# Performance work log

Hardware: AMD Instinct MI355X
Metric: run time of the kernel (lower is better)

The kernel has to match this reference:

```python
import jax, jax.numpy as jnp
import numpy as np

OUT_H, OUT_W = 7, 7
SPATIAL_SCALE = 0.25
SAMPLING_RATIO = 2


def setup_inputs() -> dict:
    key = jax.random.key(0)
    kf, kb, kc, ks = jax.random.split(key, 4)
    B, C, H, W = 2, 256, 200, 200
    N, IMG = 1000, 800.0
    features = jax.random.normal(kf, (B, C, H, W), jnp.float32)
    bidx = jax.random.randint(kb, (N,), 0, B).astype(jnp.float32)
    ctr = jax.random.uniform(kc, (N, 2)) * IMG            # box centers in image coords
    size = jax.random.uniform(ks, (N, 2)) * 256.0 + 16.0  # box sizes 16..272 px
    x1y1 = jnp.clip(ctr - size / 2, 0.0, IMG)
    x2y2 = jnp.clip(ctr + size / 2, 0.0, IMG)
    rois = jnp.concatenate(
        [bidx[:, None], x1y1[:, 0:1], x1y1[:, 1:2], x2y2[:, 0:1], x2y2[:, 1:2]], axis=1
    )
    return {"features": features, "rois": rois}


def _roi_align(features, rois):
    # torchvision.ops.roi_align semantics (aligned=False), fully vectorized over ROIs.
    B, C, H, W = features.shape
    N = rois.shape[0]
    ph, pw, ratio, scale = OUT_H, OUT_W, SAMPLING_RATIO, SPATIAL_SCALE
    b = rois[:, 0].astype(jnp.int32)
    x1, y1, x2, y2 = (rois[:, i] * scale for i in (1, 2, 3, 4))
    roi_w = jnp.maximum(x2 - x1, 1.0)
    roi_h = jnp.maximum(y2 - y1, 1.0)
    bin_w = roi_w / pw
    bin_h = roi_h / ph
    # sample coordinate s within bin p: y1 + (p*ratio + i + 0.5) * bin_h / ratio
    sy = jnp.arange(ph * ratio, dtype=features.dtype)
    sx = jnp.arange(pw * ratio, dtype=features.dtype)
    y = y1[:, None] + (sy[None, :] + 0.5) * (bin_h[:, None] / ratio)  # (N, Sy)
    x = x1[:, None] + (sx[None, :] + 0.5) * (bin_w[:, None] / ratio)  # (N, Sx)
    valid = ((y >= -1.0) & (y <= float(H)))[:, :, None] & \
            ((x >= -1.0) & (x <= float(W)))[:, None, :]               # (N, Sy, Sx)
    yc = jnp.clip(y, 0.0, H - 1.0)
    xc = jnp.clip(x, 0.0, W - 1.0)
    y0 = jnp.floor(yc).astype(jnp.int32)
    x0 = jnp.floor(xc).astype(jnp.int32)
    y1i = jnp.minimum(y0 + 1, H - 1)
    x1i = jnp.minimum(x0 + 1, W - 1)
    ly = (yc - y0)[:, :, None, None]  # (N, Sy, 1, 1)
    lx = (xc - x0)[:, None, :, None]  # (N, 1, Sx, 1)
    hy, hx = 1.0 - ly, 1.0 - lx

    def gather(yi, xi):
        # advanced indexing -> (N, Sy, Sx, C)
        return features[b[:, None, None], :, yi[:, :, None], xi[:, None, :]]

    val = (hy * hx * gather(y0, x0) + hy * lx * gather(y0, x1i)
           + ly * hx * gather(y1i, x0) + ly * lx * gather(y1i, x1i))
    val = jnp.where(valid[..., None], val, 0.0)
    val = val.reshape(N, ph, ratio, pw, ratio, C).mean(axis=(2, 4))  # avg sampling points
    return val.transpose(0, 3, 1, 2)  # (N, C, ph, pw)


def reference(features, rois):
    return _roi_align(features, rois)
```

## Files before the change

kernel.cpp:

```cpp
#include <hip/hip_runtime.h>
#include <hip/hip_fp16.h>

#define OUT_H 7
#define OUT_W 7
#define NPOS  49
#define RATIO 2
#define SCALE 0.25f
#define CCH 256
#define FH 200
#define FW 200
#define FHW (FH * FW)
#define LROW 68
#define TROW 72

struct __align__(16) H8 { __half2 h[4]; };

__device__ __forceinline__ void acc8(float (&a)[8], const H8& v, float w) {
    #pragma unroll
    for (int k = 0; k < 4; ++k) {
        a[2*k]   = fmaf(__low2float(v.h[k]),  w, a[2*k]);
        a[2*k+1] = fmaf(__high2float(v.h[k]), w, a[2*k+1]);
    }
}

__device__ __forceinline__ uint32_t part1by1(uint32_t x) {
    x &= 0xFFu;
    x = (x | (x << 4)) & 0x0F0Fu;
    x = (x | (x << 2)) & 0x3333u;
    x = (x | (x << 1)) & 0x5555u;
    return x;
}

__global__ __launch_bounds__(256) void transpose_sort(
    const float* __restrict__ in, __half* __restrict__ outT,
    const float* __restrict__ rois, uint32_t* __restrict__ perm,
    int N, int B)
{
    __shared__ __align__(16) char smem[64 * TROW * 2];
    int bid = blockIdx.x;
    int tid = threadIdx.x;

    if (bid == 0) {
        uint64_t* keys = (uint64_t*)smem;
        if (N <= 1024) {
            for (int i = tid; i < 1024; i += 256) {
                uint64_t key = ~0ull;
                if (i < N) {
                    const float* r = rois + (size_t)i * 5;
                    int bb = (int)r[0];
                    float cx = 0.5f * (r[1] + r[3]) * SCALE;
                    float cy = 0.5f * (r[2] + r[4]) * SCALE;
                    uint32_t ix = (uint32_t)fminf(fmaxf(cx, 0.f), 255.f);
                    uint32_t iy = (uint32_t)fminf(fmaxf(cy, 0.f), 255.f);
                    uint32_t m = (part1by1(iy) << 1) | part1by1(ix) | ((uint32_t)bb << 16);
                    key = ((uint64_t)m << 32) | (uint32_t)i;
                }
                keys[i] = key;
            }
            __syncthreads();
            for (int sz = 2; sz <= 1024; sz <<= 1) {
                for (int j = sz >> 1; j > 0; j >>= 1) {
                    for (int i = tid; i < 1024; i += 256) {
                        int ixj = i ^ j;
                        if (ixj > i) {
                            uint64_t a = keys[i], c = keys[ixj];
                            bool asc = ((i & sz) == 0);
                            if ((a > c) == asc) { keys[i] = c; keys[ixj] = a; }
                        }
                    }
                    __syncthreads();
                }
            }
            for (int i = tid; i < N; i += 256) perm[i] = (uint32_t)keys[i];
        } else {
            for (int i = tid; i < N; i += 256) perm[i] = (uint32_t)i;
        }
        return;
    }

    bid -= 1;
    int pt   = bid % 625;
    int rest = bid / 625;
    int ct   = rest & 3;
    int b    = rest >> 2;

    ushort* T = (ushort*)smem;
    int px0 = pt * 64, c0 = ct * 64;
    int c_l = tid >> 2;
    int pxg = (tid & 3) << 4;

    const float* src = in + ((size_t)b * CCH + c0 + c_l) * FHW + px0 + pxg;
    #pragma unroll
    for (int k = 0; k < 4; ++k) {
        float4 v = *(const float4*)(src + 4 * k);
        T[(pxg + 4*k + 0) * TROW + c_l] = __half_as_ushort(__float2half(v.x));
        T[(pxg + 4*k + 1) * TROW + c_l] = __half_as_ushort(__float2half(v.y));
        T[(pxg + 4*k + 2) * TROW + c_l] = __half_as_ushort(__float2half(v.z));
        T[(pxg + 4*k + 3) * TROW + c_l] = __half_as_ushort(__float2half(v.w));
    }
    __syncthreads();

    char* dstB = (char*)(outT + ((size_t)b * FHW + px0) * CCH + c0);
    #pragma unroll
    for (int j2 = 0; j2 < 2; ++j2) {
        int unit = tid + 256 * j2;
        int pl = unit >> 3;
        int o8 = unit & 7;
        uint4 val = *(const uint4*)&T[pl * TROW + o8 * 8];
        *(uint4*)(dstB + (size_t)pl * (CCH * 2) + o8 * 16) = val;
    }
}

__global__ __launch_bounds__(256) void roi_gather_v5(
    const __half* __restrict__ featT,
    const float* __restrict__ rois,
    const uint32_t* __restrict__ perm,
    float* __restrict__ out,
    int N)
{
    int nblk = gridDim.x;
    int wg = (nblk % 8 == 0)
           ? ((blockIdx.x & 7) * (nblk >> 3) + (blockIdx.x >> 3))
           : blockIdx.x;
    int n  = (int)perm[wg >> 2];
    int cq = wg & 3;
    int tid = threadIdx.x;
    int wave = tid >> 6, lane = tid & 63;
    int g = lane >> 3;
    int l = lane & 7;

    __shared__ float lds[NPOS * LROW];

    const float* r = rois + (size_t)n * 5;
    int   b  = (int)r[0];
    float x1 = r[1] * SCALE, y1 = r[2] * SCALE;
    float roi_w = fmaxf(r[3] * SCALE - x1, 1.0f);
    float roi_h = fmaxf(r[4] * SCALE - y1, 1.0f);
    float step_x = roi_w * (1.0f / (OUT_W * RATIO));
    float step_y = roi_h * (1.0f / (OUT_H * RATIO));

    const char* base = (const char*)featT + (size_t)b * ((size_t)FHW * CCH * 2);
    const uint32_t laneoff = (uint32_t)(cq * 64 + l * 8) * 2;

    #pragma unroll 1
    for (int rnd = 0; rnd < 2; ++rnd) {
        int p = rnd * 32 + wave * 8 + g;
        if (p < NPOS) {
            int ph = p / OUT_W;
            int pw = p - ph * OUT_W;
            float acc[8];
            #pragma unroll
            for (int k = 0; k < 8; ++k) acc[k] = 0.0f;

            #pragma unroll
            for (int iy = 0; iy < RATIO; ++iy) {
                float yy = y1 + ((float)(ph * RATIO + iy) + 0.5f) * step_y;
                bool  vy = (yy >= -1.0f) && (yy <= (float)FH);
                float yc = fminf(fmaxf(yy, 0.0f), (float)(FH - 1));
                int   yi0 = (int)yc;
                float ly = yc - (float)yi0, hy = 1.0f - ly;
                uint32_t row0  = (uint32_t)yi0 * (FW * CCH * 2);
                uint32_t rstep = (yi0 < FH - 1) ? (FW * CCH * 2) : 0u;

                #pragma unroll
                for (int ix = 0; ix < RATIO; ++ix) {
                    float xx = x1 + ((float)(pw * RATIO + ix) + 0.5f) * step_x;
                    bool  vx = (xx >= -1.0f) && (xx <= (float)FW);
                    float xc = fminf(fmaxf(xx, 0.0f), (float)(FW - 1));
                    int   xi0 = (int)xc;
                    float lx = xc - (float)xi0, hx = 1.0f - lx;
                    uint32_t dx = (xi0 < FW - 1) ? (CCH * 2) : 0u;

                    float vm  = (vy && vx) ? 0.25f : 0.0f;
                    float hyv = hy * vm, lyv = ly * vm;

                    uint32_t o00 = row0 + (uint32_t)xi0 * (CCH * 2) + laneoff;
                    H8 v00 = *(const H8*)(base + o00);
                    H8 v01 = *(const H8*)(base + o00 + dx);
                    H8 v10 = *(const H8*)(base + o00 + rstep);
                    H8 v11 = *(const H8*)(base + o00 + rstep + dx);

                    acc8(acc, v00, hyv * hx);
                    acc8(acc, v01, hyv * lx);
                    acc8(acc, v10, lyv * hx);
                    acc8(acc, v11, lyv * lx);
                }
            }
            float* lp = &lds[p * LROW + l * 8];
            *(float4*)lp       = make_float4(acc[0], acc[1], acc[2], acc[3]);
            *(float4*)(lp + 4) = make_float4(acc[4], acc[5], acc[6], acc[7]);
        }
    }
    __syncthreads();

    float* oblk = out + ((size_t)n * CCH + cq * 64) * NPOS;
    #pragma unroll 1
    for (int o = tid; o < 64 * NPOS; o += 256) {
        int c = o / NPOS;
        int p = o - c * NPOS;
        __builtin_nontemporal_store(lds[p * LROW + c], &oblk[o]);
    }
}

__global__ __launch_bounds__(256) void roi_align_kernel(
    const float* __restrict__ feat, const float* __restrict__ rois,
    float* __restrict__ out, int N, int C, int H, int W)
{
    int idx = blockIdx.x * blockDim.x + threadIdx.x;
    int total = N * C * OUT_H * OUT_W;
    if (idx >= total) return;
    int pw = idx % OUT_W;
    int ph = (idx / OUT_W) % OUT_H;
    int c  = (idx / (OUT_W * OUT_H)) % C;
    int n  = idx / (OUT_W * OUT_H * C);
    const float* r = rois + (size_t)n * 5;
    int   b  = (int)r[0];
    float x1 = r[1] * SCALE, y1 = r[2] * SCALE;
    float roi_w = fmaxf(r[3] * SCALE - x1, 1.0f);
    float roi_h = fmaxf(r[4] * SCALE - y1, 1.0f);
    float step_y = roi_h * (1.0f / (OUT_H * RATIO));
    float step_x = roi_w * (1.0f / (OUT_W * RATIO));
    const float* fptr = feat + ((size_t)b * C + c) * (size_t)(H * W);
    float acc = 0.0f;
    #pragma unroll
    for (int iy = 0; iy < RATIO; ++iy) {
        float y = y1 + ((float)(ph * RATIO + iy) + 0.5f) * step_y;
        bool vy = (y >= -1.0f) && (y <= (float)H);
        float ycl = fminf(fmaxf(y, 0.0f), (float)(H - 1));
        int y0 = (int)floorf(ycl), y1i = min(y0 + 1, H - 1);
        float ly = ycl - (float)y0, hy = 1.0f - ly;
        #pragma unroll
        for (int ix = 0; ix < RATIO; ++ix) {
            float x = x1 + ((float)(pw * RATIO + ix) + 0.5f) * step_x;
            bool vx = (x >= -1.0f) && (x <= (float)W);
            float xcl = fminf(fmaxf(x, 0.0f), (float)(W - 1));
            int x0 = (int)floorf(xcl), x1i = min(x0 + 1, W - 1);
            float lx = xcl - (float)x0, hx = 1.0f - lx;
            const float* row0 = fptr + (size_t)y0 * W;
            const float* row1 = fptr + (size_t)y1i * W;
            float v = hy * hx * row0[x0] + hy * lx * row0[x1i]
                    + ly * hx * row1[x0] + ly * lx * row1[x1i];
            acc += (vy && vx) ? v : 0.0f;
        }
    }
    out[idx] = acc * (1.0f / (RATIO * RATIO));
}

extern "C" void kernel_launch(void* const* d_in, const int* in_sizes, int n_in,
                              void* d_out, int out_size, void* d_ws, size_t ws_size,
                              hipStream_t stream) {
    const float* feat = (const float*)d_in[0];
    const float* rois = (const float*)d_in[1];
    float* out = (float*)d_out;

    const int N = in_sizes[1] / 5;
    const int B = in_sizes[0] / (CCH * FHW);

    size_t featTBytes = (size_t)B * FHW * CCH * sizeof(__half);
    size_t need = featTBytes + (size_t)N * sizeof(uint32_t);
    if (ws_size >= need) {
        __half* featT = (__half*)d_ws;
        uint32_t* perm = (uint32_t*)((char*)d_ws + featTBytes);
        transpose_sort<<<B * 4 * 625 + 1, 256, 0, stream>>>(
            feat, featT, rois, perm, N, B);
        roi_gather_v5<<<4 * N, 256, 0, stream>>>(featT, rois, perm, out, N);
    } else {
        int total = N * CCH * OUT_H * OUT_W;
        roi_align_kernel<<<(total + 255) / 256, 256, 0, stream>>>(
            feat, rois, out, N, CCH, FH, FW);
    }
}
```

Baseline: 68.12 us.

## Replace bitonic ROI sort with bucket sort, reorder gather by channel quarter

Replaces the 1024-element bitonic sort of Morton keys with a counting-sort into 64 coarse spatial buckets (batch × 4×4 grid), which removes many barrier-separated passes from block 0. The gather kernel now maps blocks channel-quarter-major (all ROIs for one channel quarter before the next), so concurrently running blocks touch a narrower slice of the transposed feature map and may reuse L2 better. The transpose also uses nontemporal loads for the fp32 input. The coarser ordering loses fine spatial locality, and atomics make the order within a bucket nondeterministic.

Measured after the change: 64.50 us. 5.3% less time.

```diff
diff --git a/kernel.cpp b/kernel.cpp
--- a/kernel.cpp
+++ b/kernel.cpp
@@ -13,6 +13,8 @@
 #define LROW 68
 #define TROW 72
 
+typedef float vfloat4 __attribute__((ext_vector_type(4)));
+
 struct __align__(16) H8 { __half2 h[4]; };
 
 __device__ __forceinline__ void acc8(float (&a)[8], const H8& v, float w) {
@@ -21,14 +23,6 @@
         a[2*k]   = fmaf(__low2float(v.h[k]),  w, a[2*k]);
         a[2*k+1] = fmaf(__high2float(v.h[k]), w, a[2*k+1]);
     }
-}
-
-__device__ __forceinline__ uint32_t part1by1(uint32_t x) {
-    x &= 0xFFu;
-    x = (x | (x << 4)) & 0x0F0Fu;
-    x = (x | (x << 2)) & 0x3333u;
-    x = (x | (x << 1)) & 0x5555u;
-    return x;
 }
 
 __global__ __launch_bounds__(256) void transpose_sort(
@@ -41,37 +35,34 @@
     int tid = threadIdx.x;
 
     if (bid == 0) {
-        uint64_t* keys = (uint64_t*)smem;
-        if (N <= 1024) {
-            for (int i = tid; i < 1024; i += 256) {
-                uint64_t key = ~0ull;
-                if (i < N) {
-                    const float* r = rois + (size_t)i * 5;
-                    int bb = (int)r[0];
-                    float cx = 0.5f * (r[1] + r[3]) * SCALE;
-                    float cy = 0.5f * (r[2] + r[4]) * SCALE;
-                    uint32_t ix = (uint32_t)fminf(fmaxf(cx, 0.f), 255.f);
-                    uint32_t iy = (uint32_t)fminf(fmaxf(cy, 0.f), 255.f);
-                    uint32_t m = (part1by1(iy) << 1) | part1by1(ix) | ((uint32_t)bb << 16);
-                    key = ((uint64_t)m << 32) | (uint32_t)i;
-                }
-                keys[i] = key;
-            }
+        unsigned char* key8 = (unsigned char*)smem;
+        int* bcnt = (int*)(smem + 4096);
+        int* bpos = (int*)(smem + 4096 + 256);
+        if (N <= 2048 && B <= 4) {
+            for (int i = tid; i < 64; i += 256) bcnt[i] = 0;
             __syncthreads();
-            for (int sz = 2; sz <= 1024; sz <<= 1) {
-                for (int j = sz >> 1; j > 0; j >>= 1) {
-                    for (int i = tid; i < 1024; i += 256) {
-                        int ixj = i ^ j;
-                        if (ixj > i) {
-                            uint64_t a = keys[i], c = keys[ixj];
-                            bool asc = ((i & sz) == 0);
-                            if ((a > c) == asc) { keys[i] = c; keys[ixj] = a; }
-                        }
-                    }
-                    __syncthreads();
-                }
-            }
-            for (int i = tid; i < N; i += 256) perm[i] = (uint32_t)keys[i];
+            for (int i = tid; i < N; i += 256) {
+                const float* r = rois + (size_t)i * 5;
+                int bb = min(max((int)r[0], 0), B - 1);
+                float cx = 0.5f * (r[1] + r[3]) * SCALE;
+                float cy = 0.5f * (r[2] + r[4]) * SCALE;
+                int gx = min(3, max(0, (int)(cx * (4.0f / FW))));
+                int gy = min(3, max(0, (int)(cy * (4.0f / FH))));
+                int m = ((gx & 1) | ((gy & 1) << 1) | ((gx >> 1) << 2) | ((gy >> 1) << 3));
+                int k = (bb << 4) | m;
+                key8[i] = (unsigned char)k;
+                atomicAdd(&bcnt[k], 1);
+            }
+            __syncthreads();
+            if (tid == 0) {
+                int s = 0;
+                for (int k = 0; k < 64; ++k) { bpos[k] = s; s += bcnt[k]; }
+            }
+            __syncthreads();
+            for (int i = tid; i < N; i += 256) {
+                int pos = atomicAdd(&bpos[key8[i]], 1);
+                perm[pos] = (uint32_t)i;
+            }
         } else {
             for (int i = tid; i < N; i += 256) perm[i] = (uint32_t)i;
         }
@@ -92,7 +83,7 @@
     const float* src = in + ((size_t)b * CCH + c0 + c_l) * FHW + px0 + pxg;
     #pragma unroll
     for (int k = 0; k < 4; ++k) {
-        float4 v = *(const float4*)(src + 4 * k);
+        vfloat4 v = __builtin_nontemporal_load((const vfloat4*)(src + 4 * k));
         T[(pxg + 4*k + 0) * TROW + c_l] = __half_as_ushort(__float2half(v.x));
         T[(pxg + 4*k + 1) * TROW + c_l] = __half_as_ushort(__float2half(v.y));
         T[(pxg + 4*k + 2) * TROW + c_l] = __half_as_ushort(__float2half(v.z));
@@ -111,7 +102,7 @@
     }
 }
 
-__global__ __launch_bounds__(256) void roi_gather_v5(
+__global__ __launch_bounds__(256) void roi_gather_v6(
     const __half* __restrict__ featT,
     const float* __restrict__ rois,
     const uint32_t* __restrict__ perm,
@@ -122,8 +113,9 @@
     int wg = (nblk % 8 == 0)
            ? ((blockIdx.x & 7) * (nblk >> 3) + (blockIdx.x >> 3))
            : blockIdx.x;
-    int n  = (int)perm[wg >> 2];
-    int cq = wg & 3;
+    int cq = wg / N;
+    int si = wg - cq * N;
+    int n  = (int)perm[si];
     int tid = threadIdx.x;
     int wave = tid >> 6, lane = tid & 63;
     int g = lane >> 3;
@@ -263,7 +255,7 @@
         uint32_t* perm = (uint32_t*)((char*)d_ws + featTBytes);
         transpose_sort<<<B * 4 * 625 + 1, 256, 0, stream>>>(
             feat, featT, rois, perm, N, B);
-        roi_gather_v5<<<4 * N, 256, 0, stream>>>(featT, rois, perm, out, N);
+        roi_gather_v6<<<4 * N, 256, 0, stream>>>(featT, rois, perm, out, N);
     } else {
         int total = N * CCH * OUT_H * OUT_W;
         roi_align_kernel<<<(total + 255) / 256, 256, 0, stream>>>(
```
